# Kernel tuning notes

Hardware: AMD Instinct MI355X
Metric: run time of the kernel (lower is better)

## Reference

```python
import jax, jax.numpy as jnp
import numpy as np

MIN_NORM = 1e-5
PROJ_EPS = 4e-3  # geoopt poincare ball boundary eps


def expmap0(u, c):
    # exponential map at origin of the Poincare ball: tanh(sqrt(c)||u||) * u / (sqrt(c)||u||)
    sqrt_c = jnp.sqrt(c)
    u_norm = jnp.maximum(jnp.linalg.norm(u, axis=-1, keepdims=True), MIN_NORM)
    return jnp.tanh(sqrt_c * u_norm) * u / (sqrt_c * u_norm)


def project(x, c):
    # clip points to stay strictly inside the ball of radius (1-eps)/sqrt(c)
    norm = jnp.maximum(jnp.linalg.norm(x, axis=-1, keepdims=True), MIN_NORM)
    maxnorm = (1.0 - PROJ_EPS) / jnp.sqrt(c)
    return jnp.where(norm > maxnorm, x / norm * maxnorm, x)


def setup_inputs() -> dict:
    key = jax.random.key(0)
    k1, k2, k3 = jax.random.split(key, 3)
    n, m, d = 4096, 4096, 1024
    query = jax.random.normal(k1, (n, d), dtype=jnp.float32)
    context = jax.random.normal(k2, (m, d), dtype=jnp.float32)
    W = jax.random.normal(k3, (d, d), dtype=jnp.float32) / np.sqrt(d)  # linear_in weight
    c = jnp.ones((1,), dtype=jnp.float32)  # curvature parameter
    return {"query": query, "context": context, "W": W, "c": c}


def reference(query, context, W, c):
    n, d = query.shape
    q = project(expmap0(query, c), c)
    ctx = project(expmap0(context, c), c)
    q = q @ W.T                      # linear_in (no bias), [n, d]
    scores = q @ ctx.T               # [n, m]
    attn = jax.nn.softmax(scores / d, axis=1)
    attn = project(expmap0(attn, c), c)
    return attn
```

## Files before the change

kernel.cpp:

```cpp
#include <hip/hip_runtime.h>
#include <cstdint>


typedef unsigned short ushort_t;
typedef __bf16 bf16x8 __attribute__((ext_vector_type(8)));
typedef float f32x4 __attribute__((ext_vector_type(4)));

__device__ __forceinline__ unsigned short f32_to_bf16(float f) {
  unsigned int u = __float_as_uint(f);
  u = (u + 0x7fffu + ((u >> 16) & 1u)) >> 16;
  return (unsigned short)u;
}

__device__ __forceinline__ void async_copy16(const void* g, void* s) {
  __builtin_amdgcn_global_load_lds(
      (const __attribute__((address_space(1))) void*)g,
      (__attribute__((address_space(3))) void*)s, 16, 0, 0);
}

__global__ void prep_rows(const float* __restrict__ q, const float* __restrict__ ctx,
                          const float* __restrict__ W, ushort_t* __restrict__ qn,
                          ushort_t* __restrict__ cn, ushort_t* __restrict__ Wb,
                          const float* __restrict__ cptr, int n, int m) {
  const int b = blockIdx.x;
  const int tid = threadIdx.x;

  if (b >= n + m) {
    int i = (b - n - m) * 256 + tid;
    float4 v = reinterpret_cast<const float4*>(W)[i];
    reinterpret_cast<ushort4*>(Wb)[i] =
        make_ushort4(f32_to_bf16(v.x), f32_to_bf16(v.y), f32_to_bf16(v.z), f32_to_bf16(v.w));
    return;
  }

  const int lane = tid & 63, w = tid >> 6;
  __shared__ float red[4];
  const float* x = (b < n) ? q + (size_t)b * 1024 : ctx + (size_t)(b - n) * 1024;
  ushort_t* out = (b < n) ? qn + (size_t)b * 1024 : cn + (size_t)(b - n) * 1024;

  float4 v = reinterpret_cast<const float4*>(x)[tid];
  float ss = v.x * v.x + v.y * v.y + v.z * v.z + v.w * v.w;
#pragma unroll
  for (int o = 32; o; o >>= 1) ss += __shfl_down(ss, o, 64);
  if (lane == 0) red[w] = ss;
  __syncthreads();
  ss = red[0] + red[1] + red[2] + red[3];

  const float c = *cptr;
  const float sqrtc = sqrtf(c);
  const float norm = fmaxf(sqrtf(ss), 1e-5f);
  const float t = tanhf(sqrtc * norm) / (sqrtc * norm);
  const float en = fmaxf(t * norm, 1e-5f);
  const float maxn = (1.0f - 4e-3f) / sqrtc;
  const float s = t * (en > maxn ? maxn / en : 1.0f);

  reinterpret_cast<ushort4*>(out)[tid] =
      make_ushort4(f32_to_bf16(v.x * s), f32_to_bf16(v.y * s),
                   f32_to_bf16(v.z * s), f32_to_bf16(v.w * s));
}

__global__ void gemm_qw(const ushort_t* __restrict__ A,
                        const ushort_t* __restrict__ B,
                        ushort_t* __restrict__ Cb, int K, int N) {
  __shared__ __align__(16) ushort_t As[128 * 32];
  __shared__ __align__(16) ushort_t Bs[64 * 32];

  const int tid = threadIdx.x;
  const int w = tid >> 6;
  const int lane = tid & 63;
  const int lane15 = lane & 15;
  const int quad = lane >> 4;
  const int wr = w >> 1, wc = w & 1;

  const size_t rowBase = (size_t)blockIdx.x * 128;
  const size_t colBase = (size_t)blockIdx.y * 64;

  const int srow = lane >> 2;
  const int scolE = (lane & 3) * 8;
  const ushort_t* Ag = A + (rowBase + (size_t)(w * 32 + srow)) * K + scolE;
  const ushort_t* Bg = B + (colBase + (size_t)(w * 16 + srow)) * K + scolE;
  ushort_t* AsD = &As[w * 1024];
  ushort_t* BsD = &Bs[w * 512];

  f32x4 acc[4][2];
#pragma unroll
  for (int i = 0; i < 4; ++i)
#pragma unroll
    for (int j = 0; j < 2; ++j) acc[i][j] = f32x4{0.f, 0.f, 0.f, 0.f};

  for (int k0 = 0; k0 < K; k0 += 32) {
    async_copy16(Ag + k0, AsD);
    async_copy16(Ag + (size_t)16 * K + k0, AsD + 512);
    async_copy16(Bg + k0, BsD);
    __syncthreads();

    bf16x8 af[4], bv[2];
#pragma unroll
    for (int i = 0; i < 4; ++i)
      af[i] = *reinterpret_cast<const bf16x8*>(&As[(wr * 64 + i * 16 + lane15) * 32 + quad * 8]);
#pragma unroll
    for (int j = 0; j < 2; ++j)
      bv[j] = *reinterpret_cast<const bf16x8*>(&Bs[(wc * 32 + j * 16 + lane15) * 32 + quad * 8]);
#pragma unroll
    for (int i = 0; i < 4; ++i)
#pragma unroll
      for (int j = 0; j < 2; ++j)
        acc[i][j] = __builtin_amdgcn_mfma_f32_16x16x32_bf16(af[i], bv[j], acc[i][j], 0, 0, 0);
    __syncthreads();
  }

#pragma unroll
  for (int i = 0; i < 4; ++i)
#pragma unroll
    for (int j = 0; j < 2; ++j)
#pragma unroll
      for (int r = 0; r < 4; ++r) {
        size_t row = rowBase + (size_t)(wr * 64 + i * 16 + quad * 4 + r);
        size_t col = colBase + (size_t)(wc * 32 + j * 16 + lane15);
        Cb[row * N + col] = f32_to_bf16(acc[i][j][r]);
      }
}


#define LDF(base, off) \
  (*reinterpret_cast<const bf16x8*>(reinterpret_cast<const char*>(base) + (off)))

#define SUBTILE(BUF, DOSTAGE, K0S)                                                        \
  do {                                                                                    \
    const ushort_t* As_ = &As[BUF][0];                                                    \
    const ushort_t* Bs_ = &Bs[BUF][0];                                                    \
    bf16x8 a0[4], b0[4], a1[4], c0[4], c1[4], b1[4];                                      \
    _Pragma("unroll") for (int mi = 0; mi < 4; ++mi) a0[mi] = LDF(As_, aO0 + mi * 2048);  \
    _Pragma("unroll") for (int ni = 0; ni < 4; ++ni) b0[ni] = LDF(Bs_, bO0 + ni * 2048);  \
    __builtin_amdgcn_s_setprio(1);                                                        \
    _Pragma("unroll") for (int mi = 0; mi < 4; ++mi)                                      \
      _Pragma("unroll") for (int ni = 0; ni < 4; ++ni)                                    \
        acc[mi][ni] = __builtin_amdgcn_mfma_f32_16x16x32_bf16(a0[mi], b0[ni], acc[mi][ni], 0, 0, 0); \
    __builtin_amdgcn_s_setprio(0);                                                        \
    _Pragma("unroll") for (int mi = 0; mi < 4; ++mi) a1[mi] = LDF(As_, aO0 + (4 + mi) * 2048); \
    _Pragma("unroll") for (int mi = 0; mi < 4; ++mi) c0[mi] = LDF(As_, aO1 + mi * 2048);  \
    _Pragma("unroll") for (int mi = 0; mi < 4; ++mi) c1[mi] = LDF(As_, aO1 + (4 + mi) * 2048); \
    _Pragma("unroll") for (int ni = 0; ni < 4; ++ni) b1[ni] = LDF(Bs_, bO1 + ni * 2048);  \
    __builtin_amdgcn_s_setprio(1);                                                        \
    _Pragma("unroll") for (int mi = 0; mi < 4; ++mi)                                      \
      _Pragma("unroll") for (int ni = 0; ni < 4; ++ni)                                    \
        acc[4 + mi][ni] = __builtin_amdgcn_mfma_f32_16x16x32_bf16(a1[mi], b0[ni], acc[4 + mi][ni], 0, 0, 0); \
    __builtin_amdgcn_s_setprio(0);                                                        \
    asm volatile("s_waitcnt lgkmcnt(0)" ::: "memory");      \
    __builtin_amdgcn_sched_barrier(0);                                                    \
    __builtin_amdgcn_s_barrier();                          \
    if (DOSTAGE) {                      \
      async_copy16(Ag + (size_t)(K0S), &As[BUF][w * 512]);                                \
      async_copy16(Ag + (size_t)64 * K + (K0S), &As[BUF][4096 + w * 512]);                \
      async_copy16(Ag + (size_t)128 * K + (K0S), &As[BUF][8192 + w * 512]);               \
      async_copy16(Ag + (size_t)192 * K + (K0S), &As[BUF][12288 + w * 512]);              \
    }                                                                                     \
    __builtin_amdgcn_s_setprio(1);                                                        \
    _Pragma("unroll") for (int mi = 0; mi < 4; ++mi)                                      \
      _Pragma("unroll") for (int ni = 0; ni < 4; ++ni)                                    \
        acc[mi][ni] = __builtin_amdgcn_mfma_f32_16x16x32_bf16(c0[mi], b1[ni], acc[mi][ni], 0, 0, 0); \
    __builtin_amdgcn_s_setprio(0);                                                        \
    if (DOSTAGE) {                      \
      async_copy16(Bg + (size_t)(K0S), &Bs[BUF][w * 512]);                                \
      async_copy16(Bg + (size_t)64 * K + (K0S), &Bs[BUF][4096 + w * 512]);                \
      async_copy16(Bg + (size_t)128 * K + (K0S), &Bs[BUF][8192 + w * 512]);               \
      async_copy16(Bg + (size_t)192 * K + (K0S), &Bs[BUF][12288 + w * 512]);              \
    }                                                                                     \
    __builtin_amdgcn_s_setprio(1);                                                        \
    _Pragma("unroll") for (int mi = 0; mi < 4; ++mi)                                      \
      _Pragma("unroll") for (int ni = 0; ni < 4; ++ni)                                    \
        acc[4 + mi][ni] = __builtin_amdgcn_mfma_f32_16x16x32_bf16(c1[mi], b1[ni], acc[4 + mi][ni], 0, 0, 0); \
    __builtin_amdgcn_s_setprio(0);                                                        \
  } while (0)

__global__ __launch_bounds__(512) void gemm_sc(const ushort_t* __restrict__ A,
                                               const ushort_t* __restrict__ B,
                                               ushort_t* __restrict__ Sb, int K, int N) {
  __shared__ __align__(16) ushort_t As[2][16384];
  __shared__ __align__(16) ushort_t Bs[2][16384];

  const int tid = threadIdx.x;
  const int w = tid >> 6;
  const int lane = tid & 63;
  const int l15 = lane & 15;
  const int quad = lane >> 4;
  const int wm = w >> 2;
  const int wn = w & 3;

  const size_t rowBase = (size_t)blockIdx.x * 256;
  const size_t colBase = (size_t)blockIdx.y * 256;

  const int colsw = (((lane & 7) ^ ((lane >> 3) & 7)) * 8);
  const ushort_t* Ag = A + (rowBase + (size_t)(w * 8 + (lane >> 3))) * K + colsw;
  const ushort_t* Bg = B + (colBase + (size_t)(w * 8 + (lane >> 3))) * K + colsw;

  const int axor = (l15 & 7) << 4;
  const int aO0 = (((wm * 128 + l15) * 128) + 0 * 64 + quad * 16) ^ axor;
  const int aO1 = (((wm * 128 + l15) * 128) + 1 * 64 + quad * 16) ^ axor;
  const int bO0 = (((wn * 64 + l15) * 128) + 0 * 64 + quad * 16) ^ axor;
  const int bO1 = (((wn * 64 + l15) * 128) + 1 * 64 + quad * 16) ^ axor;

  f32x4 acc[8][4];
#pragma unroll
  for (int mi = 0; mi < 8; ++mi)
#pragma unroll
    for (int ni = 0; ni < 4; ++ni) acc[mi][ni] = f32x4{0.f, 0.f, 0.f, 0.f};

#pragma unroll
  for (int hk = 0; hk < 4; ++hk)
    async_copy16(Ag + (size_t)(hk * 64) * K, &As[0][hk * 4096 + w * 512]);
#pragma unroll
  for (int hk = 0; hk < 4; ++hk)
    async_copy16(Bg + (size_t)(hk * 64) * K, &Bs[0][hk * 4096 + w * 512]);
#pragma unroll
  for (int hk = 0; hk < 4; ++hk)
    async_copy16(Ag + (size_t)(hk * 64) * K + 64, &As[1][hk * 4096 + w * 512]);
#pragma unroll
  for (int hk = 0; hk < 4; ++hk)
    async_copy16(Bg + (size_t)(hk * 64) * K + 64, &Bs[1][hk * 4096 + w * 512]);
  asm volatile("s_waitcnt vmcnt(8)" ::: "memory");
  __builtin_amdgcn_s_barrier();

  for (int i = 0; i < 8; ++i) {
    const bool st = (i < 7);
    const int k0s = i * 128 + 128;
    SUBTILE(0, st, k0s);
    if (st) { asm volatile("s_waitcnt vmcnt(8)" ::: "memory"); }
    else    { asm volatile("s_waitcnt vmcnt(0)" ::: "memory"); }
    __builtin_amdgcn_s_barrier();
    SUBTILE(1, st, k0s + 64);
    if (st) {
      asm volatile("s_waitcnt vmcnt(8)" ::: "memory");
      __builtin_amdgcn_s_barrier();
    }
  }

#pragma unroll
  for (int mi = 0; mi < 8; ++mi)
#pragma unroll
    for (int ni = 0; ni < 4; ++ni)
#pragma unroll
      for (int r = 0; r < 4; ++r) {
        size_t row = rowBase + (size_t)(wm * 128 + mi * 16 + quad * 4 + r);
        size_t col = colBase + (size_t)(wn * 64 + ni * 16 + l15);
        Sb[row * N + col] = f32_to_bf16(acc[mi][ni][r]);
      }
}

__global__ void softmax_hyp(const ushort_t* __restrict__ S, float* __restrict__ out,
                            const float* __restrict__ cptr, float invd) {
  const int tid = threadIdx.x;
  const int lane = tid & 63, w = tid >> 6;
  __shared__ float redS[4], redQ[4];
  const ushort_t* rp = S + (size_t)blockIdx.x * 4096;
  float* op = out + (size_t)blockIdx.x * 4096;

  float e[16];
  float sum = 0.f, sq = 0.f;
#pragma unroll
  for (int i = 0; i < 2; ++i) {
    uint4 u = reinterpret_cast<const uint4*>(rp)[i * 256 + tid];
    unsigned int uw[4] = {u.x, u.y, u.z, u.w};
#pragma unroll
    for (int k = 0; k < 4; ++k) {
      float lo = __uint_as_float(uw[k] << 16);
      float hi = __uint_as_float(uw[k] & 0xffff0000u);
      float elo = __expf(lo * invd);
      float ehi = __expf(hi * invd);
      e[i * 8 + k * 2] = elo;
      e[i * 8 + k * 2 + 1] = ehi;
      sum += elo + ehi;
      sq += elo * elo + ehi * ehi;
    }
  }
#pragma unroll
  for (int o = 32; o; o >>= 1) {
    sum += __shfl_down(sum, o, 64);
    sq += __shfl_down(sq, o, 64);
  }
  if (lane == 0) { redS[w] = sum; redQ[w] = sq; }
  __syncthreads();
  sum = redS[0] + redS[1] + redS[2] + redS[3];
  sq = redQ[0] + redQ[1] + redQ[2] + redQ[3];

  const float c = *cptr;
  const float sqrtc = sqrtf(c);
  const float anorm = sqrtf(sq) / sum;
  const float an = fmaxf(anorm, 1e-5f);
  const float t = tanhf(sqrtc * an) / (sqrtc * an);
  const float pn = fmaxf(t * anorm, 1e-5f);
  const float maxn = (1.0f - 4e-3f) / sqrtc;
  const float g = t * (pn > maxn ? maxn / pn : 1.0f) / sum;

#pragma unroll
  for (int i = 0; i < 2; ++i)
#pragma unroll
    for (int k = 0; k < 2; ++k) {
      float4 o = make_float4(e[i * 8 + k * 4] * g, e[i * 8 + k * 4 + 1] * g,
                             e[i * 8 + k * 4 + 2] * g, e[i * 8 + k * 4 + 3] * g);
      reinterpret_cast<float4*>(op)[(i * 256 + tid) * 2 + k] = o;
    }
}

extern "C" void kernel_launch(void* const* d_in, const int* in_sizes, int n_in,
                              void* d_out, int out_size, void* d_ws, size_t ws_size,
                              hipStream_t stream) {
  const float* query = (const float*)d_in[0];
  const float* context = (const float*)d_in[1];
  const float* W = (const float*)d_in[2];
  const float* cptr = (const float*)d_in[3];

  const int d = 1024;
  const int n = in_sizes[0] / d;
  const int m = in_sizes[1] / d;

  ushort_t* cn = (ushort_t*)d_ws;
  ushort_t* qw = cn + (size_t)m * d;
  ushort_t* qn = qw + (size_t)n * d;
  ushort_t* Wb = qn + (size_t)n * d;
  ushort_t* scoresB = qn;
  float* attn = (float*)d_out;

  prep_rows<<<n + m + d * d / 1024, 256, 0, stream>>>(query, context, W, qn, cn, Wb, cptr, n, m);
  gemm_qw<<<dim3(n / 128, d / 64), 256, 0, stream>>>(qn, Wb, qw, d, d);
  gemm_sc<<<dim3(n / 256, m / 256), 512, 0, stream>>>(qw, cn, scoresB, d, m);
  softmax_hyp<<<n, 256, 0, stream>>>(scoresB, attn, cptr, 1.0f / (float)d);
}
```

Baseline: 166.1 us.

## Move context normalization into the Q·W GEMM launch to overlap with compute

The prep kernel now normalizes only the query rows and converts W. The context row normalization is appended as extra blocks to the Q·W GEMM launch, using a 1D grid, so the memory-bound context prep can run alongside the compute-bound GEMM blocks. This shortens the serial prep phase at the cost of heterogeneous blocks in one launch, which may compete for CU resources and LDS.

```diff
diff --git a/kernel.cpp b/kernel.cpp
--- a/kernel.cpp
+++ b/kernel.cpp
@@ -18,15 +18,14 @@
       (__attribute__((address_space(3))) void*)s, 16, 0, 0);
 }
 
-__global__ void prep_rows(const float* __restrict__ q, const float* __restrict__ ctx,
-                          const float* __restrict__ W, ushort_t* __restrict__ qn,
-                          ushort_t* __restrict__ cn, ushort_t* __restrict__ Wb,
-                          const float* __restrict__ cptr, int n, int m) {
+__global__ void prep_q(const float* __restrict__ q, const float* __restrict__ W,
+                       ushort_t* __restrict__ qn, ushort_t* __restrict__ Wb,
+                       const float* __restrict__ cptr, int n) {
   const int b = blockIdx.x;
   const int tid = threadIdx.x;
 
-  if (b >= n + m) {
-    int i = (b - n - m) * 256 + tid;
+  if (b >= n) {
+    int i = (b - n) * 256 + tid;
     float4 v = reinterpret_cast<const float4*>(W)[i];
     reinterpret_cast<ushort4*>(Wb)[i] =
         make_ushort4(f32_to_bf16(v.x), f32_to_bf16(v.y), f32_to_bf16(v.z), f32_to_bf16(v.w));
@@ -35,8 +34,8 @@
 
   const int lane = tid & 63, w = tid >> 6;
   __shared__ float red[4];
-  const float* x = (b < n) ? q + (size_t)b * 1024 : ctx + (size_t)(b - n) * 1024;
-  ushort_t* out = (b < n) ? qn + (size_t)b * 1024 : cn + (size_t)(b - n) * 1024;
+  const float* x = q + (size_t)b * 1024;
+  ushort_t* out = qn + (size_t)b * 1024;
 
   float4 v = reinterpret_cast<const float4*>(x)[tid];
   float ss = v.x * v.x + v.y * v.y + v.z * v.z + v.w * v.w;
@@ -59,21 +58,55 @@
                    f32_to_bf16(v.z * s), f32_to_bf16(v.w * s));
 }
 
-__global__ void gemm_qw(const ushort_t* __restrict__ A,
-                        const ushort_t* __restrict__ B,
-                        ushort_t* __restrict__ Cb, int K, int N) {
+__global__ void qw_ctx(const ushort_t* __restrict__ A,
+                       const ushort_t* __restrict__ B,
+                       ushort_t* __restrict__ Cb,
+                       const float* __restrict__ ctx, ushort_t* __restrict__ cn,
+                       const float* __restrict__ cptr, int K, int N, int nGemm) {
   __shared__ __align__(16) ushort_t As[128 * 32];
   __shared__ __align__(16) ushort_t Bs[64 * 32];
 
   const int tid = threadIdx.x;
+
+  if (blockIdx.x >= nGemm) {
+    const int r = blockIdx.x - nGemm;
+    const int lane = tid & 63, wv = tid >> 6;
+    float* red = reinterpret_cast<float*>(As);
+    const float* x = ctx + (size_t)r * 1024;
+    ushort_t* out = cn + (size_t)r * 1024;
+
+    float4 v = reinterpret_cast<const float4*>(x)[tid];
+    float ss = v.x * v.x + v.y * v.y + v.z * v.z + v.w * v.w;
+#pragma unroll
+    for (int o = 32; o; o >>= 1) ss += __shfl_down(ss, o, 64);
+    if (lane == 0) red[wv] = ss;
+    __syncthreads();
+    ss = red[0] + red[1] + red[2] + red[3];
+
+    const float c = *cptr;
+    const float sqrtc = sqrtf(c);
+    const float norm = fmaxf(sqrtf(ss), 1e-5f);
+    const float t = tanhf(sqrtc * norm) / (sqrtc * norm);
+    const float en = fmaxf(t * norm, 1e-5f);
+    const float maxn = (1.0f - 4e-3f) / sqrtc;
+    const float s = t * (en > maxn ? maxn / en : 1.0f);
+
+    reinterpret_cast<ushort4*>(out)[tid] =
+        make_ushort4(f32_to_bf16(v.x * s), f32_to_bf16(v.y * s),
+                     f32_to_bf16(v.z * s), f32_to_bf16(v.w * s));
+    return;
+  }
+
+  const int gx = blockIdx.x & 31;
+  const int gy = blockIdx.x >> 5;
   const int w = tid >> 6;
   const int lane = tid & 63;
   const int lane15 = lane & 15;
   const int quad = lane >> 4;
   const int wr = w >> 1, wc = w & 1;
 
-  const size_t rowBase = (size_t)blockIdx.x * 128;
-  const size_t colBase = (size_t)blockIdx.y * 64;
+  const size_t rowBase = (size_t)gx * 128;
+  const size_t colBase = (size_t)gy * 64;
 
   const int srow = lane >> 2;
   const int scolE = (lane & 3) * 8;
@@ -321,8 +354,10 @@
   ushort_t* scoresB = qn;
   float* attn = (float*)d_out;
 
-  prep_rows<<<n + m + d * d / 1024, 256, 0, stream>>>(query, context, W, qn, cn, Wb, cptr, n, m);
-  gemm_qw<<<dim3(n / 128, d / 64), 256, 0, stream>>>(qn, Wb, qw, d, d);
+  const int nGemm = (n / 128) * (d / 64);
+
+  prep_q<<<n + d * d / 1024, 256, 0, stream>>>(query, W, qn, Wb, cptr, n);
+  qw_ctx<<<nGemm + m, 256, 0, stream>>>(qn, Wb, qw, context, cn, cptr, d, d, nGemm);
   gemm_sc<<<dim3(n / 256, m / 256), 512, 0, stream>>>(qw, cn, scoresB, d, m);
   softmax_hyp<<<n, 256, 0, stream>>>(scoresB, attn, cptr, 1.0f / (float)d);
 }
```

New measurement: 165.6 us. About the same (-0.3%).

## Fuse prep, both GEMMs and softmax into one persistent kernel with grid barriers

Applied to the files above, without the earlier changes.

Replaces the four kernel launches with a single persistent 256-block kernel. It runs normalization, the QW GEMM, the score GEMM and the hyperbolic softmax as phases separated by an atomic grid barrier. The aim is to remove launch overhead and per-kernel tail gaps. In exchange it relies on all blocks being co-resident, and the QW GEMM phase now runs with two half-blocks per CU, which may reduce parallelism.

```diff
diff --git a/kernel.cpp b/kernel.cpp
--- a/kernel.cpp
+++ b/kernel.cpp
@@ -5,6 +5,8 @@
 typedef unsigned short ushort_t;
 typedef __bf16 bf16x8 __attribute__((ext_vector_type(8)));
 typedef float f32x4 __attribute__((ext_vector_type(4)));
+
+__device__ unsigned g_bar = 0;
 
 __device__ __forceinline__ unsigned short f32_to_bf16(float f) {
   unsigned int u = __float_as_uint(f);
@@ -18,109 +20,18 @@
       (__attribute__((address_space(3))) void*)s, 16, 0, 0);
 }
 
-__global__ void prep_rows(const float* __restrict__ q, const float* __restrict__ ctx,
-                          const float* __restrict__ W, ushort_t* __restrict__ qn,
-                          ushort_t* __restrict__ cn, ushort_t* __restrict__ Wb,
-                          const float* __restrict__ cptr, int n, int m) {
-  const int b = blockIdx.x;
-  const int tid = threadIdx.x;
-
-  if (b >= n + m) {
-    int i = (b - n - m) * 256 + tid;
-    float4 v = reinterpret_cast<const float4*>(W)[i];
-    reinterpret_cast<ushort4*>(Wb)[i] =
-        make_ushort4(f32_to_bf16(v.x), f32_to_bf16(v.y), f32_to_bf16(v.z), f32_to_bf16(v.w));
-    return;
-  }
-
-  const int lane = tid & 63, w = tid >> 6;
-  __shared__ float red[4];
-  const float* x = (b < n) ? q + (size_t)b * 1024 : ctx + (size_t)(b - n) * 1024;
-  ushort_t* out = (b < n) ? qn + (size_t)b * 1024 : cn + (size_t)(b - n) * 1024;
-
-  float4 v = reinterpret_cast<const float4*>(x)[tid];
-  float ss = v.x * v.x + v.y * v.y + v.z * v.z + v.w * v.w;
-#pragma unroll
-  for (int o = 32; o; o >>= 1) ss += __shfl_down(ss, o, 64);
-  if (lane == 0) red[w] = ss;
+__device__ __forceinline__ void grid_barrier() {
   __syncthreads();
-  ss = red[0] + red[1] + red[2] + red[3];
-
-  const float c = *cptr;
-  const float sqrtc = sqrtf(c);
-  const float norm = fmaxf(sqrtf(ss), 1e-5f);
-  const float t = tanhf(sqrtc * norm) / (sqrtc * norm);
-  const float en = fmaxf(t * norm, 1e-5f);
-  const float maxn = (1.0f - 4e-3f) / sqrtc;
-  const float s = t * (en > maxn ? maxn / en : 1.0f);
-
-  reinterpret_cast<ushort4*>(out)[tid] =
-      make_ushort4(f32_to_bf16(v.x * s), f32_to_bf16(v.y * s),
-                   f32_to_bf16(v.z * s), f32_to_bf16(v.w * s));
-}
-
-__global__ void gemm_qw(const ushort_t* __restrict__ A,
-                        const ushort_t* __restrict__ B,
-                        ushort_t* __restrict__ Cb, int K, int N) {
-  __shared__ __align__(16) ushort_t As[128 * 32];
-  __shared__ __align__(16) ushort_t Bs[64 * 32];
-
-  const int tid = threadIdx.x;
-  const int w = tid >> 6;
-  const int lane = tid & 63;
-  const int lane15 = lane & 15;
-  const int quad = lane >> 4;
-  const int wr = w >> 1, wc = w & 1;
-
-  const size_t rowBase = (size_t)blockIdx.x * 128;
-  const size_t colBase = (size_t)blockIdx.y * 64;
-
-  const int srow = lane >> 2;
-  const int scolE = (lane & 3) * 8;
-  const ushort_t* Ag = A + (rowBase + (size_t)(w * 32 + srow)) * K + scolE;
-  const ushort_t* Bg = B + (colBase + (size_t)(w * 16 + srow)) * K + scolE;
-  ushort_t* AsD = &As[w * 1024];
-  ushort_t* BsD = &Bs[w * 512];
-
-  f32x4 acc[4][2];
-#pragma unroll
-  for (int i = 0; i < 4; ++i)
-#pragma unroll
-    for (int j = 0; j < 2; ++j) acc[i][j] = f32x4{0.f, 0.f, 0.f, 0.f};
-
-  for (int k0 = 0; k0 < K; k0 += 32) {
-    async_copy16(Ag + k0, AsD);
-    async_copy16(Ag + (size_t)16 * K + k0, AsD + 512);
-    async_copy16(Bg + k0, BsD);
-    __syncthreads();
-
-    bf16x8 af[4], bv[2];
-#pragma unroll
-    for (int i = 0; i < 4; ++i)
-      af[i] = *reinterpret_cast<const bf16x8*>(&As[(wr * 64 + i * 16 + lane15) * 32 + quad * 8]);
-#pragma unroll
-    for (int j = 0; j < 2; ++j)
-      bv[j] = *reinterpret_cast<const bf16x8*>(&Bs[(wc * 32 + j * 16 + lane15) * 32 + quad * 8]);
-#pragma unroll
-    for (int i = 0; i < 4; ++i)
-#pragma unroll
-      for (int j = 0; j < 2; ++j)
-        acc[i][j] = __builtin_amdgcn_mfma_f32_16x16x32_bf16(af[i], bv[j], acc[i][j], 0, 0, 0);
-    __syncthreads();
-  }
-
-#pragma unroll
-  for (int i = 0; i < 4; ++i)
-#pragma unroll
-    for (int j = 0; j < 2; ++j)
-#pragma unroll
-      for (int r = 0; r < 4; ++r) {
-        size_t row = rowBase + (size_t)(wr * 64 + i * 16 + quad * 4 + r);
-        size_t col = colBase + (size_t)(wc * 32 + j * 16 + lane15);
-        Cb[row * N + col] = f32_to_bf16(acc[i][j][r]);
-      }
-}
-
+  if (threadIdx.x == 0) {
+    unsigned old = __hip_atomic_fetch_add(&g_bar, 1u, __ATOMIC_ACQ_REL,
+                                          __HIP_MEMORY_SCOPE_AGENT);
+    unsigned tgt = (old & ~255u) + 256u;
+    while (__hip_atomic_load(&g_bar, __ATOMIC_ACQUIRE,
+                             __HIP_MEMORY_SCOPE_AGENT) < tgt)
+      __builtin_amdgcn_s_sleep(2);
+  }
+  __syncthreads();
+}
 
 #define LDF(base, off) \
   (*reinterpret_cast<const bf16x8*>(reinterpret_cast<const char*>(base) + (off)))
@@ -149,7 +60,7 @@
     asm volatile("s_waitcnt lgkmcnt(0)" ::: "memory");      \
     __builtin_amdgcn_sched_barrier(0);                                                    \
     __builtin_amdgcn_s_barrier();                          \
-    if (DOSTAGE) {                      \
+    if (DOSTAGE) {                               \
       async_copy16(Ag + (size_t)(K0S), &As[BUF][w * 512]);                                \
       async_copy16(Ag + (size_t)64 * K + (K0S), &As[BUF][4096 + w * 512]);                \
       async_copy16(Ag + (size_t)128 * K + (K0S), &As[BUF][8192 + w * 512]);               \
@@ -160,7 +71,7 @@
       _Pragma("unroll") for (int ni = 0; ni < 4; ++ni)                                    \
         acc[mi][ni] = __builtin_amdgcn_mfma_f32_16x16x32_bf16(c0[mi], b1[ni], acc[mi][ni], 0, 0, 0); \
     __builtin_amdgcn_s_setprio(0);                                                        \
-    if (DOSTAGE) {                      \
+    if (DOSTAGE) {                               \
       async_copy16(Bg + (size_t)(K0S), &Bs[BUF][w * 512]);                                \
       async_copy16(Bg + (size_t)64 * K + (K0S), &Bs[BUF][4096 + w * 512]);                \
       async_copy16(Bg + (size_t)128 * K + (K0S), &Bs[BUF][8192 + w * 512]);               \
@@ -173,133 +84,251 @@
     __builtin_amdgcn_s_setprio(0);                                                        \
   } while (0)
 
-__global__ __launch_bounds__(512) void gemm_sc(const ushort_t* __restrict__ A,
-                                               const ushort_t* __restrict__ B,
-                                               ushort_t* __restrict__ Sb, int K, int N) {
+__global__ __launch_bounds__(512) void hyp_fused(
+    const float* __restrict__ query, const float* __restrict__ ctx,
+    const float* __restrict__ W, const float* __restrict__ cptr,
+    ushort_t* __restrict__ qn, ushort_t* __restrict__ cn,
+    ushort_t* __restrict__ Wb, ushort_t* __restrict__ qw,
+    ushort_t* __restrict__ scoresB, float* __restrict__ out,
+    int n, int m, int K) {
   __shared__ __align__(16) ushort_t As[2][16384];
   __shared__ __align__(16) ushort_t Bs[2][16384];
-
+  __shared__ float redF[16];
+
+  const int b = blockIdx.x;
   const int tid = threadIdx.x;
+  const int h = tid >> 8;
+  const int tidh = tid & 255;
+  const int lane = tid & 63;
   const int w = tid >> 6;
-  const int lane = tid & 63;
-  const int l15 = lane & 15;
-  const int quad = lane >> 4;
-  const int wm = w >> 2;
-  const int wn = w & 3;
-
-  const size_t rowBase = (size_t)blockIdx.x * 256;
-  const size_t colBase = (size_t)blockIdx.y * 256;
-
-  const int colsw = (((lane & 7) ^ ((lane >> 3) & 7)) * 8);
-  const ushort_t* Ag = A + (rowBase + (size_t)(w * 8 + (lane >> 3))) * K + colsw;
-  const ushort_t* Bg = B + (colBase + (size_t)(w * 8 + (lane >> 3))) * K + colsw;
-
-  const int axor = (l15 & 7) << 4;
-  const int aO0 = (((wm * 128 + l15) * 128) + 0 * 64 + quad * 16) ^ axor;
-  const int aO1 = (((wm * 128 + l15) * 128) + 1 * 64 + quad * 16) ^ axor;
-  const int bO0 = (((wn * 64 + l15) * 128) + 0 * 64 + quad * 16) ^ axor;
-  const int bO1 = (((wn * 64 + l15) * 128) + 1 * 64 + quad * 16) ^ axor;
-
-  f32x4 acc[8][4];
-#pragma unroll
-  for (int mi = 0; mi < 8; ++mi)
-#pragma unroll
-    for (int ni = 0; ni < 4; ++ni) acc[mi][ni] = f32x4{0.f, 0.f, 0.f, 0.f};
-
-#pragma unroll
-  for (int hk = 0; hk < 4; ++hk)
-    async_copy16(Ag + (size_t)(hk * 64) * K, &As[0][hk * 4096 + w * 512]);
-#pragma unroll
-  for (int hk = 0; hk < 4; ++hk)
-    async_copy16(Bg + (size_t)(hk * 64) * K, &Bs[0][hk * 4096 + w * 512]);
-#pragma unroll
-  for (int hk = 0; hk < 4; ++hk)
-    async_copy16(Ag + (size_t)(hk * 64) * K + 64, &As[1][hk * 4096 + w * 512]);
-#pragma unroll
-  for (int hk = 0; hk < 4; ++hk)
-    async_copy16(Bg + (size_t)(hk * 64) * K + 64, &Bs[1][hk * 4096 + w * 512]);
-  asm volatile("s_waitcnt vmcnt(8)" ::: "memory");
-  __builtin_amdgcn_s_barrier();
-
-  for (int i = 0; i < 8; ++i) {
-    const bool st = (i < 7);
-    const int k0s = i * 128 + 128;
-    SUBTILE(0, st, k0s);
-    if (st) { asm volatile("s_waitcnt vmcnt(8)" ::: "memory"); }
-    else    { asm volatile("s_waitcnt vmcnt(0)" ::: "memory"); }
-    __builtin_amdgcn_s_barrier();
-    SUBTILE(1, st, k0s + 64);
-    if (st) {
-      asm volatile("s_waitcnt vmcnt(8)" ::: "memory");
-      __builtin_amdgcn_s_barrier();
-    }
-  }
-
-#pragma unroll
-  for (int mi = 0; mi < 8; ++mi)
-#pragma unroll
-    for (int ni = 0; ni < 4; ++ni)
-#pragma unroll
-      for (int r = 0; r < 4; ++r) {
-        size_t row = rowBase + (size_t)(wm * 128 + mi * 16 + quad * 4 + r);
-        size_t col = colBase + (size_t)(wn * 64 + ni * 16 + l15);
-        Sb[row * N + col] = f32_to_bf16(acc[mi][ni][r]);
-      }
-}
-
-__global__ void softmax_hyp(const ushort_t* __restrict__ S, float* __restrict__ out,
-                            const float* __restrict__ cptr, float invd) {
-  const int tid = threadIdx.x;
-  const int lane = tid & 63, w = tid >> 6;
-  __shared__ float redS[4], redQ[4];
-  const ushort_t* rp = S + (size_t)blockIdx.x * 4096;
-  float* op = out + (size_t)blockIdx.x * 4096;
-
-  float e[16];
-  float sum = 0.f, sq = 0.f;
-#pragma unroll
-  for (int i = 0; i < 2; ++i) {
-    uint4 u = reinterpret_cast<const uint4*>(rp)[i * 256 + tid];
-    unsigned int uw[4] = {u.x, u.y, u.z, u.w};
-#pragma unroll
-    for (int k = 0; k < 4; ++k) {
-      float lo = __uint_as_float(uw[k] << 16);
-      float hi = __uint_as_float(uw[k] & 0xffff0000u);
-      float elo = __expf(lo * invd);
-      float ehi = __expf(hi * invd);
-      e[i * 8 + k * 2] = elo;
-      e[i * 8 + k * 2 + 1] = ehi;
-      sum += elo + ehi;
-      sq += elo * elo + ehi * ehi;
-    }
-  }
-#pragma unroll
-  for (int o = 32; o; o >>= 1) {
-    sum += __shfl_down(sum, o, 64);
-    sq += __shfl_down(sq, o, 64);
-  }
-  if (lane == 0) { redS[w] = sum; redQ[w] = sq; }
-  __syncthreads();
-  sum = redS[0] + redS[1] + redS[2] + redS[3];
-  sq = redQ[0] + redQ[1] + redQ[2] + redQ[3];
 
   const float c = *cptr;
   const float sqrtc = sqrtf(c);
-  const float anorm = sqrtf(sq) / sum;
-  const float an = fmaxf(anorm, 1e-5f);
-  const float t = tanhf(sqrtc * an) / (sqrtc * an);
-  const float pn = fmaxf(t * anorm, 1e-5f);
   const float maxn = (1.0f - 4e-3f) / sqrtc;
-  const float g = t * (pn > maxn ? maxn / pn : 1.0f) / sum;
-
-#pragma unroll
-  for (int i = 0; i < 2; ++i)
-#pragma unroll
-    for (int k = 0; k < 2; ++k) {
-      float4 o = make_float4(e[i * 8 + k * 4] * g, e[i * 8 + k * 4 + 1] * g,
-                             e[i * 8 + k * 4 + 2] * g, e[i * 8 + k * 4 + 3] * g);
-      reinterpret_cast<float4*>(op)[(i * 256 + tid) * 2 + k] = o;
+
+  {
+    const int total = n + m + (K * K) / 1024;
+    const int perBlk = total >> 8;
+    for (int it = 0; it < (perBlk >> 1); ++it) {
+      const int cku = b * perBlk + it * 2 + h;
+      float4 v;
+      float ss = 0.f;
+      const bool isRow = (cku < n + m);
+      if (isRow) {
+        const float* x = (cku < n) ? query + (size_t)cku * 1024
+                                   : ctx + (size_t)(cku - n) * 1024;
+        v = reinterpret_cast<const float4*>(x)[tidh];
+        ss = v.x * v.x + v.y * v.y + v.z * v.z + v.w * v.w;
+#pragma unroll
+        for (int o = 32; o; o >>= 1) ss += __shfl_down(ss, o, 64);
+      } else {
+        int i = (cku - n - m) * 256 + tidh;
+        v = reinterpret_cast<const float4*>(W)[i];
+      }
+      if (lane == 0) redF[w] = ss;
+      __syncthreads();
+      if (isRow) {
+        float s2 = redF[h * 4] + redF[h * 4 + 1] + redF[h * 4 + 2] + redF[h * 4 + 3];
+        const float norm = fmaxf(sqrtf(s2), 1e-5f);
+        const float t = tanhf(sqrtc * norm) / (sqrtc * norm);
+        const float en = fmaxf(t * norm, 1e-5f);
+        const float s = t * (en > maxn ? maxn / en : 1.0f);
+        ushort_t* outp = (cku < n) ? qn + (size_t)cku * 1024
+                                   : cn + (size_t)(cku - n) * 1024;
+        reinterpret_cast<ushort4*>(outp)[tidh] =
+            make_ushort4(f32_to_bf16(v.x * s), f32_to_bf16(v.y * s),
+                         f32_to_bf16(v.z * s), f32_to_bf16(v.w * s));
+      } else {
+        int i = (cku - n - m) * 256 + tidh;
+        reinterpret_cast<ushort4*>(Wb)[i] =
+            make_ushort4(f32_to_bf16(v.x), f32_to_bf16(v.y),
+                         f32_to_bf16(v.z), f32_to_bf16(v.w));
+      }
+      __syncthreads();
     }
+  }
+  grid_barrier();
+
+  {
+    const int t = 2 * b + h;
+    const int gx = t & 31;
+    const int gy = t >> 5;
+    const int w4 = (tid >> 6) & 3;
+    const int lane15 = lane & 15;
+    const int quad = lane >> 4;
+    const int wr = w4 >> 1, wc = w4 & 1;
+    const size_t rowBase = (size_t)gx * 128;
+    const size_t colBase = (size_t)gy * 64;
+    const int srow = lane >> 2;
+    const int scolE = (lane & 3) * 8;
+    const ushort_t* Ag = qn + (rowBase + (size_t)(w4 * 32 + srow)) * K + scolE;
+    const ushort_t* Bg = Wb + (colBase + (size_t)(w4 * 16 + srow)) * K + scolE;
+    ushort_t* base = &As[0][0] + (size_t)h * 6144;
+    ushort_t* AsQ = base;
+    ushort_t* BsQ = base + 4096;
+    ushort_t* AsD = AsQ + w4 * 1024;
+    ushort_t* BsD = BsQ + w4 * 512;
+
+    f32x4 acc[4][2];
+#pragma unroll
+    for (int i = 0; i < 4; ++i)
+#pragma unroll
+      for (int j = 0; j < 2; ++j) acc[i][j] = f32x4{0.f, 0.f, 0.f, 0.f};
+
+    for (int k0 = 0; k0 < K; k0 += 32) {
+      async_copy16(Ag + k0, AsD);
+      async_copy16(Ag + (size_t)16 * K + k0, AsD + 512);
+      async_copy16(Bg + k0, BsD);
+      __syncthreads();
+
+      bf16x8 af[4], bv[2];
+#pragma unroll
+      for (int i = 0; i < 4; ++i)
+        af[i] = *reinterpret_cast<const bf16x8*>(&AsQ[(wr * 64 + i * 16 + lane15) * 32 + quad * 8]);
+#pragma unroll
+      for (int j = 0; j < 2; ++j)
+        bv[j] = *reinterpret_cast<const bf16x8*>(&BsQ[(wc * 32 + j * 16 + lane15) * 32 + quad * 8]);
+#pragma unroll
+      for (int i = 0; i < 4; ++i)
+#pragma unroll
+        for (int j = 0; j < 2; ++j)
+          acc[i][j] = __builtin_amdgcn_mfma_f32_16x16x32_bf16(af[i], bv[j], acc[i][j], 0, 0, 0);
+      __syncthreads();
+    }
+
+#pragma unroll
+    for (int i = 0; i < 4; ++i)
+#pragma unroll
+      for (int j = 0; j < 2; ++j)
+#pragma unroll
+        for (int r = 0; r < 4; ++r) {
+          size_t row = rowBase + (size_t)(wr * 64 + i * 16 + quad * 4 + r);
+          size_t col = colBase + (size_t)(wc * 32 + j * 16 + lane15);
+          qw[row * K + col] = f32_to_bf16(acc[i][j][r]);
+        }
+  }
+  grid_barrier();
+
+  {
+    const int l15 = lane & 15;
+    const int quad = lane >> 4;
+    const int wm = w >> 2;
+    const int wn = w & 3;
+    const size_t rowBase = (size_t)(b & 15) * 256;
+    const size_t colBase = (size_t)(b >> 4) * 256;
+
+    const int colsw = (((lane & 7) ^ ((lane >> 3) & 7)) * 8);
+    const ushort_t* Ag = qw + (rowBase + (size_t)(w * 8 + (lane >> 3))) * K + colsw;
+    const ushort_t* Bg = cn + (colBase + (size_t)(w * 8 + (lane >> 3))) * K + colsw;
+
+    const int axor = (l15 & 7) << 4;
+    const int aO0 = (((wm * 128 + l15) * 128) + 0 * 64 + quad * 16) ^ axor;
+    const int aO1 = (((wm * 128 + l15) * 128) + 1 * 64 + quad * 16) ^ axor;
+    const int bO0 = (((wn * 64 + l15) * 128) + 0 * 64 + quad * 16) ^ axor;
+    const int bO1 = (((wn * 64 + l15) * 128) + 1 * 64 + quad * 16) ^ axor;
+
+    f32x4 acc[8][4];
+#pragma unroll
+    for (int mi = 0; mi < 8; ++mi)
+#pragma unroll
+      for (int ni = 0; ni < 4; ++ni) acc[mi][ni] = f32x4{0.f, 0.f, 0.f, 0.f};
+
+#pragma unroll
+    for (int hk = 0; hk < 4; ++hk)
+      async_copy16(Ag + (size_t)(hk * 64) * K, &As[0][hk * 4096 + w * 512]);
+#pragma unroll
+    for (int hk = 0; hk < 4; ++hk)
+      async_copy16(Bg + (size_t)(hk * 64) * K, &Bs[0][hk * 4096 + w * 512]);
+#pragma unroll
+    for (int hk = 0; hk < 4; ++hk)
+      async_copy16(Ag + (size_t)(hk * 64) * K + 64, &As[1][hk * 4096 + w * 512]);
+#pragma unroll
+    for (int hk = 0; hk < 4; ++hk)
+      async_copy16(Bg + (size_t)(hk * 64) * K + 64, &Bs[1][hk * 4096 + w * 512]);
+    asm volatile("s_waitcnt vmcnt(8)" ::: "memory");
+    __builtin_amdgcn_s_barrier();
+
+    for (int i = 0; i < 8; ++i) {
+      const bool st = (i < 7);
+      const int k0s = i * 128 + 128;
+      SUBTILE(0, st, k0s);
+      if (st) { asm volatile("s_waitcnt vmcnt(8)" ::: "memory"); }
+      else    { asm volatile("s_waitcnt vmcnt(0)" ::: "memory"); }
+      __builtin_amdgcn_s_barrier();
+      SUBTILE(1, st, k0s + 64);
+      if (st) {
+        asm volatile("s_waitcnt vmcnt(8)" ::: "memory");
+        __builtin_amdgcn_s_barrier();
+      }
+    }
+
+#pragma unroll
+    for (int mi = 0; mi < 8; ++mi)
+#pragma unroll
+      for (int ni = 0; ni < 4; ++ni)
+#pragma unroll
+        for (int r = 0; r < 4; ++r) {
+          size_t row = rowBase + (size_t)(wm * 128 + mi * 16 + quad * 4 + r);
+          size_t col = colBase + (size_t)(wn * 64 + ni * 16 + l15);
+          scoresB[row * m + col] = f32_to_bf16(acc[mi][ni][r]);
+        }
+  }
+  grid_barrier();
+
+  {
+    const float invd = 1.0f / (float)K;
+    float* redS = redF;
+    float* redQ = redF + 8;
+    for (int it = 0; it < (n >> 9); ++it) {
+      const int row = b * 16 + it * 2 + h;
+      const ushort_t* rp = scoresB + (size_t)row * m;
+      float* op = out + (size_t)row * m;
+
+      float e[16];
+      float sum = 0.f, sq = 0.f;
+#pragma unroll
+      for (int i = 0; i < 2; ++i) {
+        uint4 u = reinterpret_cast<const uint4*>(rp)[i * 256 + tidh];
+        unsigned int uw[4] = {u.x, u.y, u.z, u.w};
+#pragma unroll
+        for (int k = 0; k < 4; ++k) {
+          float lo = __uint_as_float(uw[k] << 16);
+          float hi = __uint_as_float(uw[k] & 0xffff0000u);
+          float elo = __expf(lo * invd);
+          float ehi = __expf(hi * invd);
+          e[i * 8 + k * 2] = elo;
+          e[i * 8 + k * 2 + 1] = ehi;
+          sum += elo + ehi;
+          sq += elo * elo + ehi * ehi;
+        }
+      }
+#pragma unroll
+      for (int o = 32; o; o >>= 1) {
+        sum += __shfl_down(sum, o, 64);
+        sq += __shfl_down(sq, o, 64);
+      }
+      if (lane == 0) { redS[w] = sum; redQ[w] = sq; }
+      __syncthreads();
+      sum = redS[h * 4] + redS[h * 4 + 1] + redS[h * 4 + 2] + redS[h * 4 + 3];
+      sq = redQ[h * 4] + redQ[h * 4 + 1] + redQ[h * 4 + 2] + redQ[h * 4 + 3];
+
+      const float anorm = sqrtf(sq) / sum;
+      const float an = fmaxf(anorm, 1e-5f);
+      const float t = tanhf(sqrtc * an) / (sqrtc * an);
+      const float pn = fmaxf(t * anorm, 1e-5f);
+      const float g = t * (pn > maxn ? maxn / pn : 1.0f) / sum;
+
+#pragma unroll
+      for (int i = 0; i < 2; ++i)
+#pragma unroll
+        for (int k = 0; k < 2; ++k) {
+          float4 o = make_float4(e[i * 8 + k * 4] * g, e[i * 8 + k * 4 + 1] * g,
+                                 e[i * 8 + k * 4 + 2] * g, e[i * 8 + k * 4 + 3] * g);
+          reinterpret_cast<float4*>(op)[(i * 256 + tidh) * 2 + k] = o;
+        }
+      __syncthreads();
+    }
+  }
 }
 
 extern "C" void kernel_launch(void* const* d_in, const int* in_sizes, int n_in,
@@ -321,8 +350,6 @@
   ushort_t* scoresB = qn;
   float* attn = (float*)d_out;
 
-  prep_rows<<<n + m + d * d / 1024, 256, 0, stream>>>(query, context, W, qn, cn, Wb, cptr, n, m);
-  gemm_qw<<<dim3(n / 128, d / 64), 256, 0, stream>>>(qn, Wb, qw, d, d);
-  gemm_sc<<<dim3(n / 256, m / 256), 512, 0, stream>>>(qw, cn, scoresB, d, m);
-  softmax_hyp<<<n, 256, 0, stream>>>(scoresB, attn, cptr, 1.0f / (float)d);
-}
+  hyp_fused<<<256, 512, 0, stream>>>(query, context, W, cptr, qn, cn, Wb, qw,
+                                     scoresB, attn, n, m, d);
+}
```

After: 283.8 us. 70.9% more time.
